# Optimization experiments

Measured on AMD Instinct MI355X. Metric: run time of the kernel, lower is better.

## Reference

```python
import jax, jax.numpy as jnp
import numpy as np

N_HEAD = 16
N_KV_HEAD = 4
HEAD_DIM = 64
ROPE_THETA = 10000.0
EPS = 1e-6


def _rope_cos_sin(T, D, theta):
    # matches torch: freqs_cis[t, i] = exp(1j * t * theta**(-2i/D)), i in [0, D//2)
    inv_freq = theta ** (-jnp.arange(0, D, 2, dtype=jnp.float32) / D)  # [D//2]
    freqs = jnp.arange(T, dtype=jnp.float32)[:, None] * inv_freq[None, :]  # [T, D//2]
    return jnp.cos(freqs), jnp.sin(freqs)


def _apply_rope(x, cos, sin):
    # x: [B, T, H, D]; pairs are (even, odd) along last dim, complex-multiplied by freqs_cis
    B, T, H, D = x.shape
    xr = x.reshape(B, T, H, D // 2, 2)
    xe, xo = xr[..., 0], xr[..., 1]
    c = cos[None, :, None, :]  # [1, T, 1, D//2]
    s = sin[None, :, None, :]
    oe = xe * c - xo * s
    oo = xe * s + xo * c
    return jnp.stack([oe, oo], axis=-1).reshape(B, T, H, D)


def _qk_norm(x):
    rms = jnp.sqrt(jnp.mean(x * x, axis=-1, keepdims=True) + EPS)
    return x / rms


def setup_inputs() -> dict:
    key = jax.random.key(0)
    k = jax.random.split(key, 5)
    B, T, C = 4, 2048, 1024
    sc = 1.0 / np.sqrt(C)
    return {
        "x": jax.random.normal(k[0], (B, T, C), jnp.float32),
        "wq": jax.random.normal(k[1], (N_HEAD * HEAD_DIM, C), jnp.float32) * sc,
        "wk": jax.random.normal(k[2], (N_KV_HEAD * HEAD_DIM, C), jnp.float32) * sc,
        "wv": jax.random.normal(k[3], (N_KV_HEAD * HEAD_DIM, C), jnp.float32) * sc,
        "wo": jax.random.normal(k[4], (C, N_HEAD * HEAD_DIM), jnp.float32) * sc,
    }


def reference(x, wq, wk, wv, wo):
    B, T, C = x.shape
    H, KVH, D = N_HEAD, N_KV_HEAD, HEAD_DIM
    n_rep = H // KVH

    q = (x @ wq.T).reshape(B, T, H, D)
    k = (x @ wk.T).reshape(B, T, KVH, D)
    v = (x @ wv.T).reshape(B, T, KVH, D)

    cos, sin = _rope_cos_sin(T, D, ROPE_THETA)
    q = _qk_norm(_apply_rope(q, cos, sin))
    k = _qk_norm(_apply_rope(k, cos, sin))

    # GQA expand kv heads to n_head
    k = jnp.repeat(k, n_rep, axis=2)  # [B, T, H, D]
    v = jnp.repeat(v, n_rep, axis=2)

    q = q.transpose(0, 2, 1, 3)  # [B, H, T, D]
    k = k.transpose(0, 2, 1, 3)
    v = v.transpose(0, 2, 1, 3)

    scale = 1.0 / np.sqrt(D)
    scores = jnp.einsum("bhqd,bhkd->bhqk", q, k) * scale
    causal = jnp.tril(jnp.ones((T, T), dtype=bool))
    scores = jnp.where(causal[None, None], scores, -jnp.inf)
    attn = jax.nn.softmax(scores, axis=-1)
    y = jnp.einsum("bhqk,bhkd->bhqd", attn, v)  # [B, H, T, D]
    y = y.transpose(0, 2, 1, 3).reshape(B, T, H * D)
    return y @ wo.T
```

## Files before the change

kernel.cpp:

```cpp
#include <hip/hip_runtime.h>
#include <hip/hip_bf16.h>
#include <type_traits>

typedef __attribute__((ext_vector_type(8))) __bf16 bf16x8;
typedef __attribute__((ext_vector_type(2))) float f32x2;
typedef __attribute__((ext_vector_type(4))) float f32x4;
typedef __attribute__((ext_vector_type(16))) float f32x16;

#define MFMA16(a, b, c) __builtin_amdgcn_mfma_f32_16x16x32_bf16((a), (b), (c), 0, 0, 0)
#define MFMA32(a, b, c) __builtin_amdgcn_mfma_f32_32x32x16_bf16((a), (b), (c), 0, 0, 0)

template <bool B> struct BoolC { static constexpr bool value = B; };

__device__ __forceinline__ unsigned short f2bf(float f) {
    unsigned u = __builtin_bit_cast(unsigned, f);
    u = (u + 0x7fffu + ((u >> 16) & 1u)) >> 16;
    return (unsigned short)u;
}

__device__ __forceinline__ float bf2f(unsigned short u) {
    return __builtin_bit_cast(float, (unsigned)u << 16);
}

__device__ __forceinline__ unsigned cvt_pk_bf16(float lo, float hi) {
    unsigned r;
    asm("v_cvt_pk_bf16_f32 %0, %1, %2" : "=v"(r) : "v"(lo), "v"(hi));
    return r;
}

__device__ __forceinline__ void permswap(unsigned& a, unsigned& b) {
    asm("v_permlane32_swap_b32 %0, %1" : "+v"(a), "+v"(b));
}

__device__ __forceinline__ void gll16(const void* g, void* l) {
    __builtin_amdgcn_global_load_lds((const __attribute__((address_space(1))) void*)g,
                                     (__attribute__((address_space(3))) void*)l, 16, 0, 0);
}

__global__ __launch_bounds__(256) void cvt_fused(const float4* __restrict__ x,
                                                 const float4* __restrict__ wq,
                                                 const float4* __restrict__ wk,
                                                 const float4* __restrict__ wv,
                                                 const float4* __restrict__ wo,
                                                 ushort4* __restrict__ xb,
                                                 ushort4* __restrict__ wqkvb,
                                                 ushort4* __restrict__ wob,
                                                 float2* __restrict__ tbl) {
    int i = blockIdx.x * 256 + threadIdx.x;
    if (i < 2752512) {
        const float4* src; ushort4* dst; int j;
        if (i < 2097152)      { src = x;  dst = xb;             j = i; }
        else if (i < 2359296) { src = wq; dst = wqkvb;          j = i - 2097152; }
        else if (i < 2424832) { src = wk; dst = wqkvb + 262144; j = i - 2359296; }
        else if (i < 2490368) { src = wv; dst = wqkvb + 327680; j = i - 2424832; }
        else                  { src = wo; dst = wob;            j = i - 2490368; }
        float4 v = src[j];
        ushort4 o;
        o.x = f2bf(v.x); o.y = f2bf(v.y); o.z = f2bf(v.z); o.w = f2bf(v.w);
        dst[j] = o;
    } else {
        int j = i - 2752512;
        int t = j >> 5, k = j & 31;
        float inv = powf(10000.0f, -(float)(2 * k) * (1.0f / 64.0f));
        float a = (float)t * inv;
        tbl[j] = make_float2(cosf(a), sinf(a));
    }
}

template <typename OT>
__global__ __launch_bounds__(256) void gemm_bt_t(const unsigned short* __restrict__ A,
                                                 const unsigned short* __restrict__ Bt,
                                                 OT* __restrict__ C, int M, int N, int K) {
    __shared__ unsigned short As[2][128 * 32];
    __shared__ unsigned short Bs[2][128 * 32];
    const int tid = threadIdx.x;
    const int wid = tid >> 6, lane = tid & 63;
    const size_t brow = (size_t)blockIdx.x * 128, bcol = (size_t)blockIdx.y * 128;
    const int nkt = K >> 5;

    auto stage = [&](int buf, int kt) {
#pragma unroll
        for (int j = 0; j < 2; ++j) {
            int e = (j * 256 + tid) * 8;
            int r = e >> 5, c = e & 31;
            gll16(A + (brow + r) * K + kt * 32 + c, &As[buf][e]);
        }
#pragma unroll
        for (int j = 0; j < 2; ++j) {
            int e = (j * 256 + tid) * 8;
            int r = e >> 5, c = e & 31;
            gll16(Bt + (bcol + r) * K + kt * 32 + c, &Bs[buf][e]);
        }
    };

    f32x4 acc[4][4] = {};
    const int wm = (wid >> 1) * 64, wn = (wid & 1) * 64;
    const int fr = lane & 15, fk = (lane >> 4) * 8;

    stage(0, 0);
    for (int kt = 0; kt < nkt; ++kt) {
        __syncthreads();
        if (kt + 1 < nkt) stage((kt + 1) & 1, kt + 1);
        const int buf = kt & 1;
        bf16x8 af[4], bfr[4];
#pragma unroll
        for (int i = 0; i < 4; ++i)
            af[i] = *(const bf16x8*)&As[buf][(wm + i * 16 + fr) * 32 + fk];
#pragma unroll
        for (int i = 0; i < 4; ++i)
            bfr[i] = *(const bf16x8*)&Bs[buf][(wn + i * 16 + fr) * 32 + fk];
#pragma unroll
        for (int i = 0; i < 4; ++i)
#pragma unroll
            for (int j = 0; j < 4; ++j)
                acc[i][j] = MFMA16(af[i], bfr[j], acc[i][j]);
    }

    const int orow = (lane >> 4) * 4, ocol = lane & 15;
#pragma unroll
    for (int i = 0; i < 4; ++i)
#pragma unroll
        for (int j = 0; j < 4; ++j)
#pragma unroll
            for (int r = 0; r < 4; ++r) {
                size_t idx = (brow + wm + i * 16 + orow + r) * N + (bcol + wn + j * 16 + ocol);
                if constexpr (std::is_same_v<OT, unsigned short>)
                    C[idx] = f2bf(acc[i][j][r]);
                else
                    C[idx] = acc[i][j][r];
            }
}

__global__ __launch_bounds__(256) void rope_norm(const unsigned short* __restrict__ qkvb,
                                                 const float2* __restrict__ tbl,
                                                 unsigned short* __restrict__ qb,
                                                 unsigned short* __restrict__ kb) {
    int unit = blockIdx.x * 4 + (threadIdx.x >> 6);
    int lane = threadIdx.x & 63;
    int row = unit / 20;
    int hh = unit - row * 20;
    int b = row >> 11, t = row & 2047;
    int col = (hh < 16) ? hh * 64 : 1024 + (hh - 16) * 64;
    float x = bf2f(qkvb[(size_t)row * 1536 + col + lane]);
    float partner = __shfl_xor(x, 1);
    float2 cs = tbl[t * 32 + (lane >> 1)];
    float sgn = (lane & 1) ? cs.y : -cs.y;
    float o = x * cs.x + partner * sgn;
    float ss = o * o;
#pragma unroll
    for (int off = 1; off < 64; off <<= 1) ss += __shfl_xor(ss, off);
    o = o * rsqrtf(ss * (1.0f / 64.0f) + 1e-6f);
    if (hh < 16) o *= 0.18033688f;
    unsigned short ob = f2bf(o);
    if (hh < 16)
        qb[(((size_t)(b * 16 + hh)) * 2048 + t) * 64 + lane] = ob;
    else
        kb[(((size_t)(b * 4 + (hh - 16))) * 2048 + t) * 64 + lane] = ob;
}

__global__ __launch_bounds__(256) void vtrans(const unsigned short* __restrict__ qkvb,
                                              unsigned short* __restrict__ vt) {
    __shared__ unsigned short tile[64][72];
    int bk = blockIdx.y, t0 = blockIdx.x * 64;
    int b = bk >> 2, kvh = bk & 3;
    int i = threadIdx.x >> 2, c0 = (threadIdx.x & 3) * 16;
    const unsigned short* src = qkvb + ((size_t)(b * 2048 + t0)) * 1536 + 1280 + kvh * 64;
#pragma unroll
    for (int j = 0; j < 16; ++j) tile[i][c0 + j] = src[(size_t)i * 1536 + c0 + j];
    __syncthreads();
    unsigned short* dst = vt + (size_t)bk * 64 * 2048 + (size_t)i * 2048 + t0 + c0;
#pragma unroll
    for (int j = 0; j < 16; ++j) dst[j] = tile[c0 + j][i];
}

__global__ __launch_bounds__(256) void attn_fwd(const unsigned short* __restrict__ qb,
                                                const unsigned short* __restrict__ kbuf,
                                                const unsigned short* __restrict__ vt,
                                                unsigned short* __restrict__ Pp,
                                                float* __restrict__ Lp) {
    int orig = blockIdx.x;
    int wg = (orig & 7) * 320 + (orig >> 3);
    int bh = wg / 40;
    int u = 39 - (wg - bh * 40);
    int qt, ci, nc;
    if (u < 4)       { qt = u;               ci = 0;            nc = 1; }
    else if (u < 12) { qt = 4 + ((u - 4) >> 1);  ci = (u - 4) & 1;  nc = 2; }
    else if (u < 24) { qt = 8 + (u - 12) / 3;    ci = (u - 12) % 3; nc = 3; }
    else             { qt = 12 + ((u - 24) >> 2); ci = (u - 24) & 3; nc = 4; }
    const int nkt = 2 * qt + 2;
    const int t0 = ci * nkt / nc, t1 = (ci + 1) * nkt / nc;
    const int qbase = qt * 128;

    int b = bh >> 4, h = bh & 15, kvh = h >> 2;
    int tid = threadIdx.x, wid = tid >> 6, lane = tid & 63;
    int qrow0 = qbase + wid * 32;
    const unsigned short* Q = qb + ((size_t)(b * 16 + h)) * 2048 * 64;
    const unsigned short* Kp = kbuf + ((size_t)(b * 4 + kvh)) * 2048 * 64;
    const unsigned short* Vp = vt + ((size_t)(b * 4 + kvh)) * 64 * 2048;
    const int q32 = lane & 31, hi = lane >> 5;
    const int swz = (q32 & 7) ^ ((q32 >> 3) & 3);

    __shared__ unsigned short Klds[3][4096];
    __shared__ unsigned short Vlds[3][4096];

    auto stage = [&](int buf, int kt) {
#pragma unroll
        for (int j = 0; j < 2; ++j) {
            int t = j * 256 + tid;
            int k = t >> 3, c = (t & 7) ^ (k & 7) ^ ((k >> 3) & 3);
            gll16(Kp + ((size_t)(kt * 64 + k)) * 64 + c * 8, &Klds[buf][t * 8]);
        }
#pragma unroll
        for (int j = 0; j < 2; ++j) {
            int t = j * 256 + tid;
            int d = t >> 3, c = (t & 7) ^ (d & 7) ^ ((d >> 3) & 3);
            gll16(Vp + (size_t)d * 2048 + kt * 64 + c * 8, &Vlds[buf][t * 8]);
        }
    };

    bf16x8 qf[4];
#pragma unroll
    for (int kd = 0; kd < 4; ++kd)
        qf[kd] = *(const bf16x8*)&Q[(qrow0 + q32) * 64 + kd * 16 + hi * 8];

    f32x16 accO[2] = {};
    f32x2 lr2 = {0.0f, 0.0f};
    f32x16 s0v;
#pragma unroll
    for (int i = 0; i < 16; ++i) s0v[i] = -11.54156036f;

    const int nt = t1 - t0;
    stage(0, t0);
    if (nt > 1) stage(1, t0 + 1);
    int cur = 0;
    for (int kt = t0; kt < t1; ++kt) {
        if (kt + 1 < t1) { asm volatile("s_waitcnt vmcnt(4)" ::: "memory"); }
        else             { asm volatile("s_waitcnt vmcnt(0)" ::: "memory"); }
        __builtin_amdgcn_sched_barrier(0);
        __builtin_amdgcn_s_barrier();
        if (kt + 2 < t1) stage(cur == 0 ? 2 : cur - 1, kt + 2);
        const int kb0 = kt * 64;
        if (kb0 <= qrow0 + 31) {
            f32x16 s[2] = {s0v, s0v};
            __builtin_amdgcn_s_setprio(1);
#pragma unroll
            for (int j = 0; j < 2; ++j) {
                int row = j * 32 + q32;
#pragma unroll
                for (int kd = 0; kd < 4; ++kd) {
                    bf16x8 kf = *(const bf16x8*)&Klds[cur][row * 64 + ((2 * kd + hi) ^ swz) * 8];
                    s[j] = MFMA32(kf, qf[kd], s[j]);
                }
            }
            __builtin_amdgcn_s_setprio(0);
            const int qg = qrow0 + q32;
            bf16x8 pf[4];
            auto build = [&](auto mc) {
                constexpr bool MASKED = decltype(mc)::value;
#pragma unroll
                for (int j = 0; j < 2; ++j) {
                    float p[16];
#pragma unroll
                    for (int r = 0; r < 16; ++r) {
                        float v = __builtin_exp2f(s[j][r]);
                        if (MASKED) {
                            int key = kb0 + j * 32 + (r & 3) + 8 * (r >> 2) + 4 * hi;
                            if (key > qg) v = 0.0f;
                        }
                        p[r] = v;
                    }
#pragma unroll
                    for (int i = 0; i < 8; ++i) {
                        f32x2 pp = {p[2 * i], p[2 * i + 1]};
                        asm("v_pk_add_f32 %0, %0, %1" : "+v"(lr2) : "v"(pp));
                    }
#pragma unroll
                    for (int kl = 0; kl < 2; ++kl) {
                        unsigned c0 = cvt_pk_bf16(p[8 * kl + 0], p[8 * kl + 1]);
                        unsigned c1 = cvt_pk_bf16(p[8 * kl + 4], p[8 * kl + 5]);
                        unsigned c2 = cvt_pk_bf16(p[8 * kl + 2], p[8 * kl + 3]);
                        unsigned c3 = cvt_pk_bf16(p[8 * kl + 6], p[8 * kl + 7]);
                        permswap(c0, c1);
                        permswap(c2, c3);
                        union { bf16x8 v; unsigned u[4]; } pk;
                        pk.u[0] = c0; pk.u[1] = c2; pk.u[2] = c1; pk.u[3] = c3;
                        pf[j * 2 + kl] = pk.v;
                    }
                }
            };
            if (kb0 + 63 > qrow0) build(BoolC<true>{});
            else                  build(BoolC<false>{});
            __builtin_amdgcn_s_setprio(1);
#pragma unroll
            for (int nd = 0; nd < 2; ++nd) {
                int row = nd * 32 + q32;
#pragma unroll
                for (int ks = 0; ks < 4; ++ks) {
                    bf16x8 vf = *(const bf16x8*)&Vlds[cur][row * 64 + ((2 * ks + hi) ^ swz) * 8];
                    accO[nd] = MFMA32(pf[ks], vf, accO[nd]);
                }
            }
            __builtin_amdgcn_s_setprio(0);
        }
        cur = (cur == 2) ? 0 : cur + 1;
    }

    float lrun = lr2[0] + lr2[1];
    unsigned lu = __builtin_bit_cast(unsigned, lrun);
    unsigned la = lu, lb = lu;
    permswap(la, lb);
    float L = __builtin_bit_cast(float, la) + __builtin_bit_cast(float, lb);

    unsigned short* Pw = Pp + (((size_t)bh * 40 + u) * 128 + wid * 32) * 64;
#pragma unroll
    for (int nd = 0; nd < 2; ++nd)
#pragma unroll
        for (int r = 0; r < 16; ++r) {
            int lrow = (r & 3) + 8 * (r >> 2) + 4 * hi;
            Pw[(size_t)lrow * 64 + nd * 32 + q32] = f2bf(accO[nd][r]);
        }
    if (lane < 32)
        Lp[((size_t)bh * 40 + u) * 128 + wid * 32 + q32] = L;
}

__global__ __launch_bounds__(256) void attn_fin(const unsigned short* __restrict__ Pp,
                                                const float* __restrict__ Lp,
                                                unsigned short* __restrict__ y) {
    int idx = blockIdx.x * 256 + threadIdx.x;
    int dg = idx & 15;
    int grow = idx >> 4;
    int bh = grow >> 11, t = grow & 2047;
    int b = bh >> 4, h = bh & 15;
    int qt = t >> 7;
    int bse, nc;
    if (qt < 4)       { bse = qt;                nc = 1; }
    else if (qt < 8)  { bse = 4 + 2 * (qt - 4);  nc = 2; }
    else if (qt < 12) { bse = 12 + 3 * (qt - 8); nc = 3; }
    else              { bse = 24 + 4 * (qt - 12); nc = 4; }
    float o0 = 0.f, o1 = 0.f, o2 = 0.f, o3 = 0.f, L = 0.f;
    for (int ci = 0; ci < nc; ++ci) {
        size_t slot = ((size_t)bh * 40 + bse + ci) * 128 + (t & 127);
        ushort4 pw = *(const ushort4*)&Pp[slot * 64 + dg * 4];
        o0 += bf2f(pw.x); o1 += bf2f(pw.y); o2 += bf2f(pw.z); o3 += bf2f(pw.w);
        L += Lp[slot];
    }
    float inv = 1.0f / L;
    ushort4 w;
    w.x = f2bf(o0 * inv); w.y = f2bf(o1 * inv);
    w.z = f2bf(o2 * inv); w.w = f2bf(o3 * inv);
    *(ushort4*)&y[((size_t)(b * 2048 + t)) * 1024 + h * 64 + dg * 4] = w;
}

extern "C" void kernel_launch(void* const* d_in, const int* in_sizes, int n_in,
                              void* d_out, int out_size, void* d_ws, size_t ws_size,
                              hipStream_t stream) {
    const float* x = (const float*)d_in[0];
    const float* wq = (const float*)d_in[1];
    const float* wk = (const float*)d_in[2];
    const float* wv = (const float*)d_in[3];
    const float* wo = (const float*)d_in[4];
    float* out = (float*)d_out;

    char* ws = (char*)d_ws;
    size_t off = 0;
    auto alloc = [&](size_t bytes) {
        void* p = ws + off;
        off += (bytes + 255) & ~(size_t)255;
        return p;
    };
    unsigned short* xb    = (unsigned short*)alloc(8192ull * 1024 * 2);
    unsigned short* wqkvb = (unsigned short*)alloc(1536ull * 1024 * 2);
    unsigned short* wob   = (unsigned short*)alloc(1024ull * 1024 * 2);
    char*           big   = (char*)alloc(41943040ull + 1310720ull);
    float2*         tbl   = (float2*)alloc(2048ull * 32 * 8);
    unsigned short* qb    = (unsigned short*)alloc(8192ull * 1024 * 2);
    unsigned short* kb    = (unsigned short*)alloc(4ull * 4 * 2048 * 64 * 2);
    unsigned short* vt    = (unsigned short*)alloc(4ull * 4 * 64 * 2048 * 2);

    unsigned short* qkvb  = (unsigned short*)big;
    unsigned short* Pp    = (unsigned short*)big;
    float*          Lp    = (float*)(big + 41943040ull);
    unsigned short* ybf   = xb;

    cvt_fused<<<11008, 256, 0, stream>>>((const float4*)x, (const float4*)wq, (const float4*)wk,
                                         (const float4*)wv, (const float4*)wo,
                                         (ushort4*)xb, (ushort4*)wqkvb, (ushort4*)wob, tbl);

    gemm_bt_t<unsigned short><<<dim3(64, 12), 256, 0, stream>>>(xb, wqkvb, qkvb, 8192, 1536, 1024);

    rope_norm<<<(8192 * 20) / 4, 256, 0, stream>>>(qkvb, tbl, qb, kb);

    vtrans<<<dim3(32, 16), 256, 0, stream>>>(qkvb, vt);

    attn_fwd<<<2560, 256, 0, stream>>>(qb, kb, vt, Pp, Lp);

    attn_fin<<<8192, 256, 0, stream>>>(Pp, Lp, ybf);

    gemm_bt_t<float><<<dim3(64, 8), 256, 0, stream>>>(ybf, wob, out, 8192, 1024, 1024);
}
```

Before: 188.6 us.

## Switch attention to double-buffered LDS with launch bounds for four blocks per CU

Cuts the K/V LDS ring from three stages to two, replaces the hand-tuned vmcnt waits with a plain __syncthreads before each prefetch, and requests four 256-thread blocks per CU. QK^T and softmax now run one 32-key half at a time instead of keeping both score tiles live, which lowers register pressure. The aim is higher occupancy to hide latency. The cost is a shallower prefetch, since each load now waits on the full barrier, and less overlap of MFMA work between the two score tiles.

```diff
diff --git a/kernel.cpp b/kernel.cpp
--- a/kernel.cpp
+++ b/kernel.cpp
@@ -9,8 +9,6 @@
 
 #define MFMA16(a, b, c) __builtin_amdgcn_mfma_f32_16x16x32_bf16((a), (b), (c), 0, 0, 0)
 #define MFMA32(a, b, c) __builtin_amdgcn_mfma_f32_32x32x16_bf16((a), (b), (c), 0, 0, 0)
-
-template <bool B> struct BoolC { static constexpr bool value = B; };
 
 __device__ __forceinline__ unsigned short f2bf(float f) {
     unsigned u = __builtin_bit_cast(unsigned, f);
@@ -173,11 +171,11 @@
     for (int j = 0; j < 16; ++j) dst[j] = tile[c0 + j][i];
 }
 
-__global__ __launch_bounds__(256) void attn_fwd(const unsigned short* __restrict__ qb,
-                                                const unsigned short* __restrict__ kbuf,
-                                                const unsigned short* __restrict__ vt,
-                                                unsigned short* __restrict__ Pp,
-                                                float* __restrict__ Lp) {
+__global__ __launch_bounds__(256, 4) void attn_fwd(const unsigned short* __restrict__ qb,
+                                                   const unsigned short* __restrict__ kbuf,
+                                                   const unsigned short* __restrict__ vt,
+                                                   unsigned short* __restrict__ Pp,
+                                                   float* __restrict__ Lp) {
     int orig = blockIdx.x;
     int wg = (orig & 7) * 320 + (orig >> 3);
     int bh = wg / 40;
@@ -200,8 +198,8 @@
     const int q32 = lane & 31, hi = lane >> 5;
     const int swz = (q32 & 7) ^ ((q32 >> 3) & 3);
 
-    __shared__ unsigned short Klds[3][4096];
-    __shared__ unsigned short Vlds[3][4096];
+    __shared__ unsigned short Klds[2][4096];
+    __shared__ unsigned short Vlds[2][4096];
 
     auto stage = [&](int buf, int kt) {
 #pragma unroll
@@ -229,67 +227,58 @@
 #pragma unroll
     for (int i = 0; i < 16; ++i) s0v[i] = -11.54156036f;
 
-    const int nt = t1 - t0;
     stage(0, t0);
-    if (nt > 1) stage(1, t0 + 1);
-    int cur = 0;
     for (int kt = t0; kt < t1; ++kt) {
-        if (kt + 1 < t1) { asm volatile("s_waitcnt vmcnt(4)" ::: "memory"); }
-        else             { asm volatile("s_waitcnt vmcnt(0)" ::: "memory"); }
-        __builtin_amdgcn_sched_barrier(0);
-        __builtin_amdgcn_s_barrier();
-        if (kt + 2 < t1) stage(cur == 0 ? 2 : cur - 1, kt + 2);
+        __syncthreads();
+        if (kt + 1 < t1) stage((kt + 1 - t0) & 1, kt + 1);
+        const int cur = (kt - t0) & 1;
         const int kb0 = kt * 64;
         if (kb0 <= qrow0 + 31) {
-            f32x16 s[2] = {s0v, s0v};
-            __builtin_amdgcn_s_setprio(1);
+            const int qg = qrow0 + q32;
+            const bool diag = (kb0 + 63 > qrow0);
+            bf16x8 pf[4];
 #pragma unroll
             for (int j = 0; j < 2; ++j) {
-                int row = j * 32 + q32;
+                f32x16 s = s0v;
+                const int row = j * 32 + q32;
+                __builtin_amdgcn_s_setprio(1);
 #pragma unroll
                 for (int kd = 0; kd < 4; ++kd) {
                     bf16x8 kf = *(const bf16x8*)&Klds[cur][row * 64 + ((2 * kd + hi) ^ swz) * 8];
-                    s[j] = MFMA32(kf, qf[kd], s[j]);
-                }
-            }
-            __builtin_amdgcn_s_setprio(0);
-            const int qg = qrow0 + q32;
-            bf16x8 pf[4];
-            auto build = [&](auto mc) {
-                constexpr bool MASKED = decltype(mc)::value;
-#pragma unroll
-                for (int j = 0; j < 2; ++j) {
-                    float p[16];
+                    s = MFMA32(kf, qf[kd], s);
+                }
+                __builtin_amdgcn_s_setprio(0);
+                float p[16];
+                if (diag) {
 #pragma unroll
                     for (int r = 0; r < 16; ++r) {
-                        float v = __builtin_exp2f(s[j][r]);
-                        if (MASKED) {
-                            int key = kb0 + j * 32 + (r & 3) + 8 * (r >> 2) + 4 * hi;
-                            if (key > qg) v = 0.0f;
-                        }
+                        float v = __builtin_exp2f(s[r]);
+                        int key = kb0 + j * 32 + (r & 3) + 8 * (r >> 2) + 4 * hi;
+                        if (key > qg) v = 0.0f;
                         p[r] = v;
                     }
-#pragma unroll
-                    for (int i = 0; i < 8; ++i) {
-                        f32x2 pp = {p[2 * i], p[2 * i + 1]};
-                        asm("v_pk_add_f32 %0, %0, %1" : "+v"(lr2) : "v"(pp));
-                    }
-#pragma unroll
-                    for (int kl = 0; kl < 2; ++kl) {
-                        unsigned c0 = cvt_pk_bf16(p[8 * kl + 0], p[8 * kl + 1]);
-                        unsigned c1 = cvt_pk_bf16(p[8 * kl + 4], p[8 * kl + 5]);
-                        unsigned c2 = cvt_pk_bf16(p[8 * kl + 2], p[8 * kl + 3]);
-                        unsigned c3 = cvt_pk_bf16(p[8 * kl + 6], p[8 * kl + 7]);
-                        permswap(c0, c1);
-                        permswap(c2, c3);
-                        union { bf16x8 v; unsigned u[4]; } pk;
-                        pk.u[0] = c0; pk.u[1] = c2; pk.u[2] = c1; pk.u[3] = c3;
-                        pf[j * 2 + kl] = pk.v;
-                    }
-                }
-            };
-            if (kb0 + 63 > qrow0) build(BoolC<true>{});
-            else                  build(BoolC<false>{});
+                } else {
+#pragma unroll
+                    for (int r = 0; r < 16; ++r) p[r] = __builtin_exp2f(s[r]);
+                }
+#pragma unroll
+                for (int i = 0; i < 8; ++i) {
+                    f32x2 pp = {p[2 * i], p[2 * i + 1]};
+                    asm("v_pk_add_f32 %0, %0, %1" : "+v"(lr2) : "v"(pp));
+                }
+#pragma unroll
+                for (int kl = 0; kl < 2; ++kl) {
+                    unsigned c0 = cvt_pk_bf16(p[8 * kl + 0], p[8 * kl + 1]);
+                    unsigned c1 = cvt_pk_bf16(p[8 * kl + 4], p[8 * kl + 5]);
+                    unsigned c2 = cvt_pk_bf16(p[8 * kl + 2], p[8 * kl + 3]);
+                    unsigned c3 = cvt_pk_bf16(p[8 * kl + 6], p[8 * kl + 7]);
+                    permswap(c0, c1);
+                    permswap(c2, c3);
+                    union { bf16x8 v; unsigned u[4]; } pk;
+                    pk.u[0] = c0; pk.u[1] = c2; pk.u[2] = c1; pk.u[3] = c3;
+                    pf[j * 2 + kl] = pk.v;
+                }
+            }
             __builtin_amdgcn_s_setprio(1);
 #pragma unroll
             for (int nd = 0; nd < 2; ++nd) {
@@ -302,7 +291,6 @@
             }
             __builtin_amdgcn_s_setprio(0);
         }
-        cur = (cur == 2) ? 0 : cur + 1;
     }
 
     float lrun = lr2[0] + lr2[1];
```

New measurement: 174.8 us. 1.08x faster.
